# Performance work log

Hardware: AMD Instinct MI355X
Metric: run time of the kernel (lower is better)

The kernel has to match this reference:

```python
import jax, jax.numpy as jnp
import numpy as np


def setup_inputs() -> dict:
    key = jax.random.key(0)
    k1, k2 = jax.random.split(key, 2)
    B, S, H, E = 4, 4096, 4096, 64
    h = jax.random.normal(k1, (B, S, H), dtype=jnp.float32)
    # gate weight as in nn.Linear(hidden_dim, num_experts): W [E, H], bias [E]
    W = jax.random.normal(k2, (E, H), dtype=jnp.float32) * (1.0 / np.sqrt(H))
    b = jnp.zeros((E,), dtype=jnp.float32)
    return {"h": h, "W": W, "b": b, "k": 2}


def reference(h, W, b, k):
    # eval-mode forward (self.training == False, so no gaussian noise)
    # logits: [B, S, E]
    logits = jnp.einsum('bsh,eh->bse', h, W) + b
    E = logits.shape[-1]
    B, S = h.shape[0], h.shape[1]

    # top-k over experts, softmax over the k selected logits
    topk_vals, topk_idx = jax.lax.top_k(logits, k)          # [B, S, k]
    topk_scores = jax.nn.softmax(topk_vals, axis=-1)        # [B, S, k]

    # scatter softmaxed scores back into a zero [B, S, E] tensor
    # (topk indices are distinct, so sum-of-one-hots == scatter)
    route_weights = jnp.sum(
        jax.nn.one_hot(topk_idx, E, dtype=topk_scores.dtype) * topk_scores[..., None],
        axis=-2,
    )  # [B, S, E]

    # aux-loss statistics
    importance = jax.nn.softmax(logits, axis=-1).sum(axis=(0, 1))            # [E]
    load = (route_weights > 0).astype(jnp.float32).sum(axis=(0, 1)) / (B * S)  # [E]
    aux_loss = jnp.mean(importance * load * (E ** 2))
    return route_weights, aux_loss
```

## Files before the change

### kernel.cpp

```cpp
#include <hip/hip_runtime.h>
#include <hip/hip_bf16.h>
#include <math.h>

typedef __attribute__((ext_vector_type(8))) short  short8;
typedef __attribute__((ext_vector_type(4))) float  float4v;

#define NE 64
#define FLAG_CAP 8192
#define EPS_TIE 2e-4f

__device__ __forceinline__ unsigned short f2bf(float x){
  unsigned u = __float_as_uint(x);
  return (unsigned short)((u + 0x7fffu + ((u>>16)&1u)) >> 16);
}
__device__ __forceinline__ float bf2f(unsigned short h){
  return __uint_as_float(((unsigned)h)<<16);
}
__device__ __forceinline__ float warp_sum64(float v){
  #pragma unroll
  for (int off=1; off<64; off<<=1) v += __shfl_xor(v, off, 64);
  return v;
}

__global__ __launch_bounds__(256) void prep_w(
    const float* __restrict__ W, unsigned short* __restrict__ whi,
    unsigned short* __restrict__ wlo, float* __restrict__ zbuf, int K)
{
  if (blockIdx.x == 0){
    #pragma unroll
    for (int i=0;i<5;++i){
      const int idx = threadIdx.x + i*256;
      if (idx < 1025) zbuf[idx] = 0.f;
    }
  }
  const int id = blockIdx.x*256 + threadIdx.x;
  const int nfrag = (K/32)*4*64;
  if (id >= nfrag) return;
  const int lane = id & 63, te = (id>>6)&3, ks = id>>8;
  const int e  = te*16 + (lane&15);
  const int k0 = ks*32 + ((lane>>4)<<3);
  const float* src = W + (size_t)e*K + k0;
  short8 h8, l8;
  #pragma unroll
  for (int j=0;j<8;++j){
    float x = src[j];
    unsigned short hb = f2bf(x);
    h8[j] = (short)hb;
    l8[j] = (short)f2bf(x - bf2f(hb));
  }
  const size_t off = (size_t)id*8;
  *(short8*)(whi + off) = h8;
  *(short8*)(wlo + off) = l8;
}

__device__ __forceinline__ void cvt8b(const float4& c, const float4& d,
                                      short8& hi, short8& lo){
  const float f[8] = {c.x,c.y,c.z,c.w,d.x,d.y,d.z,d.w};
  union { short8 s; unsigned u[4]; } H, L;
  #pragma unroll
  for (int p=0;p<4;++p){
    float2 v = make_float2(f[2*p], f[2*p+1]);
    __hip_bfloat162 hb = __float22bfloat162_rn(v);
    H.u[p] = *reinterpret_cast<unsigned*>(&hb);
    float2 back = __bfloat1622float2(hb);
    float2 res = make_float2(v.x - back.x, v.y - back.y);
    __hip_bfloat162 lb = __float22bfloat162_rn(res);
    L.u[p] = *reinterpret_cast<unsigned*>(&lb);
  }
  hi = H.s; lo = L.s;
}

#define MFMA3(AH, AL, BH, BL, ACC)                                          \
  ACC = __builtin_amdgcn_mfma_f32_16x16x32_bf16(AH, BH, ACC, 0,0,0);        \
  ACC = __builtin_amdgcn_mfma_f32_16x16x32_bf16(AH, BL, ACC, 0,0,0);        \
  ACC = __builtin_amdgcn_mfma_f32_16x16x32_bf16(AL, BH, ACC, 0,0,0);

__global__ __launch_bounds__(512) void gemm_router_reg(
    const float* __restrict__ hp, const unsigned short* __restrict__ whi,
    const unsigned short* __restrict__ wlo, const float* __restrict__ bp,
    float* __restrict__ outp, float* __restrict__ imp8, float* __restrict__ cnt8,
    int* __restrict__ flagCnt, int* __restrict__ flagList, int K, long M)
{
  __shared__ float part[2][4][32][64];
  __shared__ float red[2][8][64];

  const int tid = threadIdx.x;
  const int l = tid & 63, w = tid >> 6;
  const int tq = w >> 2, kq = w & 3;
  const int tok0 = blockIdx.x * 64;
  const int r16 = l & 15, kg = l >> 4;
  const int ktiles = K / 128;
  const int kbase = kq * (K/4);

  const float* a0 = hp + (size_t)(tok0 + tq*32      + r16)*K + kbase + kg*8;
  const float* a1 = hp + (size_t)(tok0 + tq*32 + 16 + r16)*K + kbase + kg*8;
  const unsigned short* bh = whi + (size_t)(kq*ktiles)*2048 + (size_t)l*8;
  const unsigned short* bl = wlo + (size_t)(kq*ktiles)*2048 + (size_t)l*8;

  float4v acc[2][4];
  #pragma unroll
  for (int m=0;m<2;++m)
    #pragma unroll
    for (int te=0;te<4;++te) acc[m][te] = (float4v){0.f,0.f,0.f,0.f};

  float4 A0[2][2], A1[2][2];
  short8 Bh0[4], Bl0[4], Bh1[4], Bl1[4];

#define LOADT(S, T) {                                            \
  const float* p0 = a0 + (size_t)(T)*32;                         \
  const float* p1 = a1 + (size_t)(T)*32;                         \
  A##S[0][0] = *(const float4*)(p0);                             \
  A##S[0][1] = *(const float4*)(p0 + 4);                         \
  A##S[1][0] = *(const float4*)(p1);                             \
  A##S[1][1] = *(const float4*)(p1 + 4);                         \
  const unsigned short* pb = bh + (size_t)(T)*2048;              \
  const unsigned short* pl = bl + (size_t)(T)*2048;              \
  _Pragma("unroll")                                              \
  for (int te=0; te<4; ++te){                                    \
    Bh##S[te] = *(const short8*)(pb + te*512);                   \
    Bl##S[te] = *(const short8*)(pl + te*512);                   \
  }                                                              \
}

#define COMPUTET(S) {                                            \
  short8 Ah0, Al0, Ah1, Al1;                                     \
  cvt8b(A##S[0][0], A##S[0][1], Ah0, Al0);                       \
  cvt8b(A##S[1][0], A##S[1][1], Ah1, Al1);                       \
  _Pragma("unroll")                                              \
  for (int te=0; te<4; ++te){                                    \
    MFMA3(Ah0, Al0, Bh##S[te], Bl##S[te], acc[0][te]);           \
    MFMA3(Ah1, Al1, Bh##S[te], Bl##S[te], acc[1][te]);           \
  }                                                              \
}

  LOADT(0, 0);
  for (int t = 0; t < ktiles-2; t += 2){
    LOADT(1, t+1);
    COMPUTET(0);
    LOADT(0, t+2);
    COMPUTET(1);
  }
  LOADT(1, ktiles-1);
  COMPUTET(0);
  COMPUTET(1);

#undef LOADT
#undef COMPUTET

  #pragma unroll
  for (int m=0;m<2;++m)
    #pragma unroll
    for (int te=0;te<4;++te)
      #pragma unroll
      for (int r=0;r<4;++r)
        part[tq][kq][m*16 + (kg<<2) + r][te*16 + r16] = acc[m][te][r];
  __syncthreads();

  const float bias = bp[l];
  float impL = 0.f, cntL = 0.f;
  #pragma unroll 1
  for (int it=0; it<8; ++it){
    const int  tl = w*8 + it;
    const long tg = (long)tok0 + tl;
    const int  tq2 = tl >> 5, rr = tl & 31;
    float v = part[tq2][0][rr][l];
    v += part[tq2][1][rr][l];
    v += part[tq2][2][rr][l];
    v += part[tq2][3][rr][l];
    v += bias;
    float m1 = v; int i1 = l;
    #pragma unroll
    for (int off=1; off<64; off<<=1){
      float ov = __shfl_xor(m1, off, 64);
      int   oi = __shfl_xor(i1, off, 64);
      if (ov > m1 || (ov == m1 && oi < i1)){ m1 = ov; i1 = oi; }
    }
    float vm = (l == i1) ? -3.4e38f : v;
    float m2 = vm; int i2 = l;
    #pragma unroll
    for (int off=1; off<64; off<<=1){
      float ov = __shfl_xor(m2, off, 64);
      int   oi = __shfl_xor(i2, off, 64);
      if (ov > m2 || (ov == m2 && oi < i2)){ m2 = ov; i2 = oi; }
    }
    float vm3 = (l==i1 || l==i2) ? -3.4e38f : v;
    float m3 = vm3;
    #pragma unroll
    for (int off=1; off<64; off<<=1) m3 = fmaxf(m3, __shfl_xor(m3, off, 64));
    if ((m2 - m3) < EPS_TIE && l == 0){
      int idx = atomicAdd(flagCnt, 1);
      if (idx < FLAG_CAP) flagList[idx] = (int)tg;
    }
    const float ex = __expf(m2 - m1);
    const float s1 = 1.f / (1.f + ex);
    const float s2 = ex * s1;
    const float p = __expf(v - m1);
    const float S = warp_sum64(p);
    impL += p / S;
    const float rw = (l==i1) ? s1 : ((l==i2) ? s2 : 0.f);
    outp[(size_t)tg*NE + l] = rw;
    if (l==i1 || l==i2) cntL += 1.f;
  }
  red[0][w][l] = impL;
  red[1][w][l] = cntL;
  __syncthreads();
  if (tid < 64){
    float s = 0.f, c = 0.f;
    #pragma unroll
    for (int q=0; q<8; ++q){ s += red[0][q][tid]; c += red[1][q][tid]; }
    const int g = (blockIdx.x & 7) << 6;
    atomicAdd(&imp8[g + tid], s);
    atomicAdd(&cnt8[g + tid], c);
  }
}

__global__ __launch_bounds__(256) void fixup_aux(
    const float* __restrict__ hp, const float* __restrict__ Wp,
    const float* __restrict__ bp, float* __restrict__ outp,
    const int* __restrict__ flagCnt, const int* __restrict__ flagList,
    const float* __restrict__ imp8, const float* __restrict__ cnt8,
    float* __restrict__ auxp, float scale, int K)
{
  __shared__ float hrow[4096];
  __shared__ float lg[NE];
  if (blockIdx.x == 0 && threadIdx.x < 64){
    float s = 0.f, c = 0.f;
    #pragma unroll
    for (int g=0; g<8; ++g){
      s += imp8[(g<<6) + threadIdx.x];
      c += cnt8[(g<<6) + threadIdx.x];
    }
    float v = s * c;
    v = warp_sum64(v);
    if (threadIdx.x == 0) auxp[0] = v * scale;
  }
  int n = *flagCnt; if (n > FLAG_CAP) n = FLAG_CAP;
  const int e   = threadIdx.x >> 2;
  const int sub = threadIdx.x & 3;
  const int lane = threadIdx.x & 63;

  for (int f = blockIdx.x; f < n; f += gridDim.x){
    const int tok = flagList[f];
    const float* hr = hp + (size_t)tok*K;
    #pragma unroll
    for (int c=0; c<4; ++c){
      const int idx = threadIdx.x*4 + c*1024;
      *(float4*)&hrow[idx] = *(const float4*)(hr + idx);
    }
    __syncthreads();
    const float* wr = Wp + (size_t)e*K;
    float s = 0.f;
    for (int it=0; it<64; ++it){
      const int k0 = it*64 + sub*16;
      #pragma unroll
      for (int u=0; u<4; ++u){
        float4 wv = *(const float4*)(wr + k0 + u*4);
        float4 hv = *(const float4*)(&hrow[k0 + u*4]);
        s = fmaf(hv.x, wv.x, s); s = fmaf(hv.y, wv.y, s);
        s = fmaf(hv.z, wv.z, s); s = fmaf(hv.w, wv.w, s);
      }
    }
    s += __shfl_xor(s, 1, 64);
    s += __shfl_xor(s, 2, 64);
    if (sub == 0) lg[e] = s + bp[e];
    __syncthreads();
    if (threadIdx.x < 64){
      const float v = lg[lane];
      float m1 = v; int i1 = lane;
      #pragma unroll
      for (int off=1; off<64; off<<=1){
        float ov = __shfl_xor(m1, off, 64);
        int   oi = __shfl_xor(i1, off, 64);
        if (ov > m1 || (ov == m1 && oi < i1)){ m1 = ov; i1 = oi; }
      }
      float vm = (lane == i1) ? -3.4e38f : v;
      float m2 = vm; int i2 = lane;
      #pragma unroll
      for (int off=1; off<64; off<<=1){
        float ov = __shfl_xor(m2, off, 64);
        int   oi = __shfl_xor(i2, off, 64);
        if (ov > m2 || (ov == m2 && oi < i2)){ m2 = ov; i2 = oi; }
      }
      const float ex = __expf(m2 - m1);
      const float s1 = 1.f / (1.f + ex);
      const float s2 = ex * s1;
      const float rw = (lane==i1) ? s1 : ((lane==i2) ? s2 : 0.f);
      outp[(size_t)tok * NE + lane] = rw;
    }
    __syncthreads();
  }
}

extern "C" void kernel_launch(void* const* d_in, const int* in_sizes, int n_in,
                              void* d_out, int out_size, void* d_ws, size_t ws_size,
                              hipStream_t stream){
  const float* hp = (const float*)d_in[0];
  const float* Wp = (const float*)d_in[1];
  const float* bp = (const float*)d_in[2];
  const int  E = in_sizes[2];
  const int  K = in_sizes[1] / E;
  const long M = (long)in_sizes[0] / K;

  float* outp = (float*)d_out;
  float* auxp = outp + (size_t)M * E;

  char* ws = (char*)d_ws;
  float* imp8     = (float*)(ws + 0);
  float* cnt8     = (float*)(ws + 2048);
  int*   flagCnt  = (int*)  (ws + 4096);
  int*   flagList = (int*)  (ws + 4160);
  unsigned short* whi = (unsigned short*)(ws + 65536);
  unsigned short* wlo = (unsigned short*)(ws + 65536 + 524288);

  const int nfragBlocks = ((K/32)*4*64 + 255)/256;

  prep_w<<<dim3(nfragBlocks), dim3(256), 0, stream>>>(Wp, whi, wlo, (float*)ws, K);
  gemm_router_reg<<<dim3((int)(M/64)), dim3(512), 0, stream>>>(hp, whi, wlo, bp, outp,
                                                               imp8, cnt8, flagCnt, flagList,
                                                               K, M);
  fixup_aux<<<dim3(128), dim3(256), 0, stream>>>(hp, Wp, bp, outp, flagCnt, flagList,
                                                 imp8, cnt8, auxp, (float)E/(float)M, K);
}
```

Before: 102.4 us.

## Shrink router GEMM blocks to 32 tokens and single-buffer weight fragments

```diff
diff --git a/kernel.cpp b/kernel.cpp
--- a/kernel.cpp
+++ b/kernel.cpp
@@ -75,25 +75,25 @@
   ACC = __builtin_amdgcn_mfma_f32_16x16x32_bf16(AH, BL, ACC, 0,0,0);        \
   ACC = __builtin_amdgcn_mfma_f32_16x16x32_bf16(AL, BH, ACC, 0,0,0);
 
-__global__ __launch_bounds__(512) void gemm_router_reg(
+__global__ __launch_bounds__(256, 4) void gemm_router_reg(
     const float* __restrict__ hp, const unsigned short* __restrict__ whi,
     const unsigned short* __restrict__ wlo, const float* __restrict__ bp,
     float* __restrict__ outp, float* __restrict__ imp8, float* __restrict__ cnt8,
     int* __restrict__ flagCnt, int* __restrict__ flagList, int K, long M)
 {
-  __shared__ float part[2][4][32][64];
-  __shared__ float red[2][8][64];
+  __shared__ float part[4][32][64];
+  __shared__ float red[2][4][64];
 
   const int tid = threadIdx.x;
   const int l = tid & 63, w = tid >> 6;
-  const int tq = w >> 2, kq = w & 3;
-  const int tok0 = blockIdx.x * 64;
+  const int kq = w;
+  const int tok0 = blockIdx.x * 32;
   const int r16 = l & 15, kg = l >> 4;
   const int ktiles = K / 128;
   const int kbase = kq * (K/4);
 
-  const float* a0 = hp + (size_t)(tok0 + tq*32      + r16)*K + kbase + kg*8;
-  const float* a1 = hp + (size_t)(tok0 + tq*32 + 16 + r16)*K + kbase + kg*8;
+  const float* a0 = hp + (size_t)(tok0      + r16)*K + kbase + kg*8;
+  const float* a1 = hp + (size_t)(tok0 + 16 + r16)*K + kbase + kg*8;
   const unsigned short* bh = whi + (size_t)(kq*ktiles)*2048 + (size_t)l*8;
   const unsigned short* bl = wlo + (size_t)(kq*ktiles)*2048 + (size_t)l*8;
 
@@ -104,21 +104,24 @@
     for (int te=0;te<4;++te) acc[m][te] = (float4v){0.f,0.f,0.f,0.f};
 
   float4 A0[2][2], A1[2][2];
-  short8 Bh0[4], Bl0[4], Bh1[4], Bl1[4];
-
-#define LOADT(S, T) {                                            \
+  short8 Bh[4], Bl[4];
+
+#define LOADA(S, T) {                                            \
   const float* p0 = a0 + (size_t)(T)*32;                         \
   const float* p1 = a1 + (size_t)(T)*32;                         \
   A##S[0][0] = *(const float4*)(p0);                             \
   A##S[0][1] = *(const float4*)(p0 + 4);                         \
   A##S[1][0] = *(const float4*)(p1);                             \
   A##S[1][1] = *(const float4*)(p1 + 4);                         \
+}
+
+#define LOADB(T) {                                               \
   const unsigned short* pb = bh + (size_t)(T)*2048;              \
   const unsigned short* pl = bl + (size_t)(T)*2048;              \
   _Pragma("unroll")                                              \
   for (int te=0; te<4; ++te){                                    \
-    Bh##S[te] = *(const short8*)(pb + te*512);                   \
-    Bl##S[te] = *(const short8*)(pl + te*512);                   \
+    Bh[te] = *(const short8*)(pb + te*512);                      \
+    Bl[te] = *(const short8*)(pl + te*512);                      \
   }                                                              \
 }
 
@@ -128,23 +131,29 @@
   cvt8b(A##S[1][0], A##S[1][1], Ah1, Al1);                       \
   _Pragma("unroll")                                              \
   for (int te=0; te<4; ++te){                                    \
-    MFMA3(Ah0, Al0, Bh##S[te], Bl##S[te], acc[0][te]);           \
-    MFMA3(Ah1, Al1, Bh##S[te], Bl##S[te], acc[1][te]);           \
+    MFMA3(Ah0, Al0, Bh[te], Bl[te], acc[0][te]);                 \
+    MFMA3(Ah1, Al1, Bh[te], Bl[te], acc[1][te]);                 \
   }                                                              \
 }
 
-  LOADT(0, 0);
-  for (int t = 0; t < ktiles-2; t += 2){
-    LOADT(1, t+1);
+  LOADA(0, 0);
+  int t = 0;
+  for (; t < ktiles-2; t += 2){
+    LOADA(1, t+1);
+    LOADB(t);
     COMPUTET(0);
-    LOADT(0, t+2);
+    LOADA(0, t+2);
+    LOADB(t+1);
     COMPUTET(1);
   }
-  LOADT(1, ktiles-1);
+  LOADA(1, t+1);
+  LOADB(t);
   COMPUTET(0);
+  LOADB(t+1);
   COMPUTET(1);
 
-#undef LOADT
+#undef LOADA
+#undef LOADB
 #undef COMPUTET
 
   #pragma unroll
@@ -153,7 +162,7 @@
     for (int te=0;te<4;++te)
       #pragma unroll
       for (int r=0;r<4;++r)
-        part[tq][kq][m*16 + (kg<<2) + r][te*16 + r16] = acc[m][te][r];
+        part[kq][m*16 + (kg<<2) + r][te*16 + r16] = acc[m][te][r];
   __syncthreads();
 
   const float bias = bp[l];
@@ -162,11 +171,10 @@
   for (int it=0; it<8; ++it){
     const int  tl = w*8 + it;
     const long tg = (long)tok0 + tl;
-    const int  tq2 = tl >> 5, rr = tl & 31;
-    float v = part[tq2][0][rr][l];
-    v += part[tq2][1][rr][l];
-    v += part[tq2][2][rr][l];
-    v += part[tq2][3][rr][l];
+    float v = part[0][tl][l];
+    v += part[1][tl][l];
+    v += part[2][tl][l];
+    v += part[3][tl][l];
     v += bias;
     float m1 = v; int i1 = l;
     #pragma unroll
@@ -207,7 +215,7 @@
   if (tid < 64){
     float s = 0.f, c = 0.f;
     #pragma unroll
-    for (int q=0; q<8; ++q){ s += red[0][q][tid]; c += red[1][q][tid]; }
+    for (int q=0; q<4; ++q){ s += red[0][q][tid]; c += red[1][q][tid]; }
     const int g = (blockIdx.x & 7) << 6;
     atomicAdd(&imp8[g + tid], s);
     atomicAdd(&cnt8[g + tid], c);
@@ -315,7 +323,7 @@
   const int nfragBlocks = ((K/32)*4*64 + 255)/256;
 
   prep_w<<<dim3(nfragBlocks), dim3(256), 0, stream>>>(Wp, whi, wlo, (float*)ws, K);
-  gemm_router_reg<<<dim3((int)(M/64)), dim3(512), 0, stream>>>(hp, whi, wlo, bp, outp,
+  gemm_router_reg<<<dim3((int)(M/32)), dim3(256), 0, stream>>>(hp, whi, wlo, bp, outp,
                                                                imp8, cnt8, flagCnt, flagList,
                                                                K, M);
   fixup_aux<<<dim3(128), dim3(256), 0, stream>>>(hp, Wp, bp, outp, flagCnt, flagList,
```

Measured after the change: 103.9 us. Within noise of the previous version (+1.4%).
